# Performance work log

Measured on AMD Instinct MI355X. Metric: run time of the kernel, lower is better.

## Reference

```python
import jax, jax.numpy as jnp
import numpy as np

L = 5          # num_layer
D = 128        # emb_dim
N = 150000     # nodes
E = 500000     # edges
NF_ATOM, VA = 9, 119   # OGB atom feature count / max vocab
NF_BOND, VB = 3, 6     # OGB bond feature count / max vocab
BN_EPS = 1e-5


def setup_inputs() -> dict:
    key = jax.random.key(0)
    ks = jax.random.split(key, 10)
    s = 0.1
    x = jax.random.randint(ks[0], (N, NF_ATOM), 0, VA)
    edge_index = jax.random.randint(ks[1], (2, E), 0, N)
    edge_attr = jax.random.randint(ks[2], (E, NF_BOND), 0, VB)
    batch = jnp.sort(jax.random.randint(ks[3], (N,), 0, 2000))
    atom_emb = s * jax.random.normal(ks[4], (NF_ATOM, VA, D), dtype=jnp.float32)
    bond_emb = s * jax.random.normal(ks[5], (L, NF_BOND, VB, D), dtype=jnp.float32)
    eps = jnp.zeros((L,), jnp.float32)
    W1 = s * jax.random.normal(ks[6], (L, D, 2 * D), dtype=jnp.float32)
    b1 = jnp.zeros((L, 2 * D), jnp.float32)
    bn1_g = jnp.ones((L, 2 * D), jnp.float32)
    bn1_b = jnp.zeros((L, 2 * D), jnp.float32)
    W2 = s * jax.random.normal(ks[7], (L, 2 * D, D), dtype=jnp.float32)
    b2 = jnp.zeros((L, D), jnp.float32)
    bn_g = jnp.ones((L, D), jnp.float32)
    bn_b = jnp.zeros((L, D), jnp.float32)
    return dict(x=x, edge_index=edge_index, edge_attr=edge_attr, batch=batch,
                atom_emb=atom_emb, bond_emb=bond_emb, eps=eps,
                W1=W1, b1=b1, bn1_g=bn1_g, bn1_b=bn1_b,
                W2=W2, b2=b2, bn_g=bn_g, bn_b=bn_b)


def _bn(z, g, b):
    # BatchNorm1d with batch statistics (training-mode normalization)
    m = jnp.mean(z, axis=0)
    v = jnp.var(z, axis=0)
    return (z - m) * jax.lax.rsqrt(v + BN_EPS) * g + b


def _sum_embed(tables, idx):
    # tables: [F, V, D], idx: [n, F] -> sum_f tables[f][idx[:, f]] -> [n, D]
    return jax.vmap(lambda t, i: t[i], in_axes=(0, 1))(tables, idx).sum(0)


def reference(x, edge_index, edge_attr, batch, atom_emb, bond_emb, eps,
              W1, b1, bn1_g, bn1_b, W2, b2, bn_g, bn_b):
    n = x.shape[0]
    src, dst = edge_index[0], edge_index[1]
    h = _sum_embed(atom_emb, x)                      # AtomEncoder: [N, D]
    for l in range(L):
        e = _sum_embed(bond_emb[l], edge_attr)       # BondEncoder: [E, D]
        msg = jax.nn.relu(h[src] + e)                # message: gather + add + ReLU
        aggr = jax.ops.segment_sum(msg, dst, num_segments=n)  # scatter-add
        z = (1.0 + eps[l]) * h + aggr
        z = z @ W1[l] + b1[l]                        # [N, 2D]
        z = jax.nn.relu(_bn(z, bn1_g[l], bn1_b[l]))
        z = z @ W2[l] + b2[l]                        # [N, D]
        z = _bn(z, bn_g[l], bn_b[l])                 # outer BatchNorm
        if l < L - 1:
            z = jax.nn.relu(z)
        # dropout is identity in eval mode
        h = z + h                                    # residual
    return h  # JK='last'
```

## Files before the change

### kernel.cpp

```cpp
#include <hip/hip_runtime.h>

#define N_NODES 150000
#define N_EDGES 500000
#define D 128
#define D2 256
#define NLAYER 5
#define NB1 586
#define NROWT 9375
#define NBLK1 512
#define NBLK2 512

typedef __attribute__((ext_vector_type(8))) short bf16x8;
typedef __attribute__((ext_vector_type(4))) float f32x4;
typedef __attribute__((ext_vector_type(2))) float f32x2;
typedef __attribute__((ext_vector_type(4))) unsigned short ushort4v;
typedef __attribute__((ext_vector_type(8))) unsigned short ushort8v;
typedef __attribute__((ext_vector_type(4))) unsigned int u32x4;

__device__ __forceinline__ unsigned short f2bf(float f) {
    unsigned int u = __builtin_bit_cast(unsigned int, f);
    u += 0x7fffu + ((u >> 16) & 1u);
    return (unsigned short)(u >> 16);
}
__device__ __forceinline__ unsigned short f2bf_hw(float f) {
    return __builtin_bit_cast(unsigned short, (__bf16)f);
}
__device__ __forceinline__ float bf2f(unsigned short s) {
    unsigned int u = ((unsigned int)s) << 16;
    return __builtin_bit_cast(float, u);
}

__global__ __launch_bounds__(256) void prepw_kernel(const float* __restrict__ W1,
        const float* __restrict__ W2, unsigned short* __restrict__ w1t,
        unsigned short* __restrict__ w2t) {
    int i = blockIdx.x * 256 + threadIdx.x;
    if (i < NLAYER * D2 * D) {
        int l = i / (D2 * D);
        int rem = i % (D2 * D);
        int n = rem / D;
        int k = rem % D;
        w1t[i] = f2bf(W1[(l * D + k) * D2 + n]);
    }
    if (i < NLAYER * D * D2) {
        int l = i / (D * D2);
        int rem = i % (D * D2);
        int n = rem / D2;
        int k = rem % D2;
        w2t[i] = f2bf(W2[(l * D2 + k) * D + n]);
    }
}

__global__ __launch_bounds__(128) void combo_kernel(const float* __restrict__ bemb,
        float* __restrict__ combo) {
    int b = blockIdx.x;
    int l = b / 216, p = b % 216;
    int a0 = p % 6, a1 = (p / 6) % 6, a2 = p / 36;
    int d = threadIdx.x;
    combo[b * D + d] = bemb[((l * 3 + 0) * 6 + a0) * D + d]
                     + bemb[((l * 3 + 1) * 6 + a1) * D + d]
                     + bemb[((l * 3 + 2) * 6 + a2) * D + d];
}

__global__ __launch_bounds__(256) void atom_enc_kernel(const int* __restrict__ x,
        const float* __restrict__ aemb, unsigned short* __restrict__ hbf) {
    int node = blockIdx.x * 8 + (threadIdx.x >> 5);
    int t = threadIdx.x & 31;
    int d0 = t * 4;
    f32x4 s = {0, 0, 0, 0};
#pragma unroll
    for (int f = 0; f < 9; ++f) {
        int xi = x[node * 9 + f];
        f32x4 v = *(const f32x4*)(aemb + (size_t)(f * 119 + xi) * D + d0);
        s[0] += v[0]; s[1] += v[1]; s[2] += v[2]; s[3] += v[3];
    }
    ushort4v o;
#pragma unroll
    for (int j = 0; j < 4; ++j) o[j] = f2bf_hw(s[j]);
    *(ushort4v*)(hbf + (size_t)node * D + d0) = o;
}

__global__ __launch_bounds__(256) void hist_kernel(const int* __restrict__ ei,
        int* __restrict__ deg) {
    int e = blockIdx.x * 256 + threadIdx.x;
    if (e < N_EDGES) atomicAdd(&deg[ei[N_EDGES + e]], 1);
}

__global__ __launch_bounds__(256) void scan1_kernel(const int* __restrict__ deg,
        int* __restrict__ part, int* __restrict__ bsum) {
    __shared__ int sd[256];
    int tid = threadIdx.x;
    int i = blockIdx.x * 256 + tid;
    int v = (i < N_NODES) ? deg[i] : 0;
    sd[tid] = v;
    __syncthreads();
    for (int off = 1; off < 256; off <<= 1) {
        int t = (tid >= off) ? sd[tid - off] : 0;
        __syncthreads();
        sd[tid] += t;
        __syncthreads();
    }
    if (i < N_NODES) part[i] = sd[tid] - v;
    if (tid == 255) bsum[blockIdx.x] = sd[255];
}

__global__ __launch_bounds__(1024) void scan2_kernel(const int* __restrict__ bsum,
        int* __restrict__ boff) {
    __shared__ int sd[1024];
    int tid = threadIdx.x;
    int v = (tid < NB1) ? bsum[tid] : 0;
    sd[tid] = v;
    __syncthreads();
    for (int off = 1; off < 1024; off <<= 1) {
        int t = (tid >= off) ? sd[tid - off] : 0;
        __syncthreads();
        sd[tid] += t;
        __syncthreads();
    }
    if (tid < NB1) boff[tid] = sd[tid] - v;
}

__global__ __launch_bounds__(256) void scan3_kernel(const int* __restrict__ part,
        const int* __restrict__ boff, int* __restrict__ row_start) {
    int i = blockIdx.x * 256 + threadIdx.x;
    if (i < N_NODES) row_start[i] = part[i] + boff[i >> 8];
}

__global__ __launch_bounds__(256) void bin_kernel(const int* __restrict__ ei,
        const int* __restrict__ ea, const int* __restrict__ row_start,
        int* __restrict__ cursor, int* __restrict__ bins) {
    int e = blockIdx.x * 256 + threadIdx.x;
    if (e >= N_EDGES) return;
    int dst = ei[N_EDGES + e];
    int pos = row_start[dst] + atomicAdd(&cursor[dst], 1);
    int pack = ea[e * 3 + 0] + ea[e * 3 + 1] * 6 + ea[e * 3 + 2] * 36;
    bins[pos] = ei[e] | (pack << 18);
}

__global__ __launch_bounds__(256) void aggr_kernel(const int* __restrict__ row_start,
        const int* __restrict__ deg, const int* __restrict__ bins,
        const float* __restrict__ combo, const unsigned short* __restrict__ hbf,
        const float* __restrict__ epsp, unsigned short* __restrict__ A) {
    int wid = threadIdx.x >> 6;
    int lane = threadIdx.x & 63;
    int sub = lane >> 4;
    int t = lane & 15;
    int d0 = t * 8;
    int node = blockIdx.x * 16 + wid * 4 + sub;
    float ke = 1.0f + epsp[0];
    int start = row_start[node];
    int dg = deg[node];
    f32x4 s0 = {0, 0, 0, 0}, s1 = {0, 0, 0, 0};
    int entry = (dg > 0) ? bins[start] : 0;
    for (int i = 0; i < dg; ++i) {
        int next = (i + 1 < dg) ? bins[start + i + 1] : 0;
        int src = entry & 0x3FFFF;
        int pack = entry >> 18;
        ushort8v hv = *(const ushort8v*)(hbf + (size_t)src * D + d0);
        f32x4 c0 = *(const f32x4*)(combo + pack * D + d0);
        f32x4 c1 = *(const f32x4*)(combo + pack * D + d0 + 4);
#pragma unroll
        for (int j = 0; j < 4; ++j) {
            s0[j] += fmaxf(bf2f(hv[j]) + c0[j], 0.f);
            s1[j] += fmaxf(bf2f(hv[j + 4]) + c1[j], 0.f);
        }
        entry = next;
    }
    ushort8v hs = *(const ushort8v*)(hbf + (size_t)node * D + d0);
    ushort8v o;
#pragma unroll
    for (int j = 0; j < 4; ++j) {
        o[j]     = f2bf_hw(ke * bf2f(hs[j]) + s0[j]);
        o[j + 4] = f2bf_hw(ke * bf2f(hs[j + 4]) + s1[j]);
    }
    *(ushort8v*)(A + (size_t)node * D + d0) = o;
}

__global__ __launch_bounds__(256) void gemm1_kernel(const unsigned short* __restrict__ A,
        const unsigned short* __restrict__ w1t, const float* __restrict__ b1,
        unsigned short* __restrict__ z1, float* __restrict__ part1) {
    __shared__ unsigned short sm[4][16][76];
    int wave = threadIdx.x >> 6;
    int lane = threadIdx.x & 63;
    int l15 = lane & 15;
    int kg = lane >> 4;
    int rrow = lane >> 3;
    int rcol = (lane & 7) * 8;

    bf16x8 B[4][4];
    float bias[4];
#pragma unroll
    for (int t = 0; t < 4; ++t) {
        int col = (wave * 4 + t) * 16 + l15;
        bias[t] = b1[col];
#pragma unroll
        for (int kk = 0; kk < 4; ++kk)
            B[t][kk] = *(const bf16x8*)(w1t + (size_t)col * D + kk * 32 + kg * 8);
    }
    float s[4] = {0.f, 0.f, 0.f, 0.f}, q[4] = {0.f, 0.f, 0.f, 0.f};

    int rt = blockIdx.x;
    bf16x8 afn[4];
    {
        int row = rt * 16 + l15;
#pragma unroll
        for (int kk = 0; kk < 4; ++kk)
            afn[kk] = *(const bf16x8*)(A + (size_t)row * D + kk * 32 + kg * 8);
    }
    while (rt < NROWT) {
        int rtn = rt + NBLK1;
        bf16x8 af[4];
#pragma unroll
        for (int kk = 0; kk < 4; ++kk) af[kk] = afn[kk];
        if (rtn < NROWT) {
            int row = rtn * 16 + l15;
#pragma unroll
            for (int kk = 0; kk < 4; ++kk)
                afn[kk] = *(const bf16x8*)(A + (size_t)row * D + kk * 32 + kg * 8);
        }
        f32x4 acc[4];
#pragma unroll
        for (int t = 0; t < 4; ++t) acc[t] = (f32x4){0.f, 0.f, 0.f, 0.f};
#pragma unroll
        for (int kk = 0; kk < 4; ++kk)
#pragma unroll
            for (int t = 0; t < 4; ++t)
                acc[t] = __builtin_amdgcn_mfma_f32_16x16x32_bf16(af[kk], B[t][kk], acc[t], 0, 0, 0);
#pragma unroll
        for (int t = 0; t < 4; ++t) {
#pragma unroll
            for (int r = 0; r < 4; ++r) {
                float va = acc[t][r] + bias[t];
                s[t] += va;
                q[t] = fmaf(va, va, q[t]);
                sm[wave][kg * 4 + r][t * 16 + l15] = f2bf_hw(va);
            }
        }
        ushort8v v0 = *(const ushort8v*)&sm[wave][rrow][rcol];
        ushort8v v1 = *(const ushort8v*)&sm[wave][8 + rrow][rcol];
        *(ushort8v*)(z1 + (size_t)(rt * 16 + rrow) * D2 + wave * 64 + rcol) = v0;
        *(ushort8v*)(z1 + (size_t)(rt * 16 + 8 + rrow) * D2 + wave * 64 + rcol) = v1;
        rt = rtn;
    }
#pragma unroll
    for (int t = 0; t < 4; ++t) {
        s[t] += __shfl_xor(s[t], 16); s[t] += __shfl_xor(s[t], 32);
        q[t] += __shfl_xor(q[t], 16); q[t] += __shfl_xor(q[t], 32);
        if (kg == 0) {
            int col = (wave * 4 + t) * 16 + l15;
            part1[(size_t)blockIdx.x * 512 + col] = s[t];
            part1[(size_t)blockIdx.x * 512 + 256 + col] = q[t];
        }
    }
}

__global__ __launch_bounds__(256) void reduce_finalize_kernel(const float* __restrict__ part,
        int nblk, int C, const float* __restrict__ g, const float* __restrict__ bb,
        float* __restrict__ scale, float* __restrict__ shift,
        unsigned short* __restrict__ shpb) {
    int c = blockIdx.x;
    int tid = threadIdx.x;
    float s = 0.f, q = 0.f;
    for (int i = tid; i < nblk; i += 256) {
        s += part[(size_t)i * 2 * C + c];
        q += part[(size_t)i * 2 * C + C + c];
    }
#pragma unroll
    for (int off = 1; off < 64; off <<= 1) {
        s += __shfl_xor(s, off);
        q += __shfl_xor(q, off);
    }
    __shared__ float rs[4], rq[4];
    int w = tid >> 6;
    if ((tid & 63) == 0) { rs[w] = s; rq[w] = q; }
    __syncthreads();
    if (tid == 0) {
        s = rs[0] + rs[1] + rs[2] + rs[3];
        q = rq[0] + rq[1] + rq[2] + rq[3];
        float inv_n = 1.0f / (float)N_NODES;
        float mean = s * inv_n;
        float var = q * inv_n - mean * mean;
        float sc = g[c] * rsqrtf(var + 1e-5f);
        float sh = bb[c] - mean * sc;
        scale[c] = sc;
        shift[c] = sh;
        shpb[c] = f2bf(sh / sc);
    }
}

__global__ __launch_bounds__(256) void gemm2_kernel(const unsigned short* __restrict__ z1,
        const float* __restrict__ scale1, const unsigned short* __restrict__ shpb,
        const unsigned short* __restrict__ w2t, const float* __restrict__ b2,
        unsigned short* __restrict__ z2, float* __restrict__ part2) {
    __shared__ unsigned short sm2[4][16][44];
    int wave = threadIdx.x >> 6;
    int lane = threadIdx.x & 63;
    int l15 = lane & 15;
    int kg = lane >> 4;
    int rrow = lane >> 2;
    int rcol = (lane & 3) * 8;

    bf16x8 B[2][8];
    float bias[2];
#pragma unroll
    for (int t = 0; t < 2; ++t) {
        int col = (wave * 2 + t) * 16 + l15;
        bias[t] = b2[col];
#pragma unroll
        for (int kk = 0; kk < 8; ++kk) {
            bf16x8 raw = *(const bf16x8*)(w2t + (size_t)col * D2 + kk * 32 + kg * 8);
            int k0 = kk * 32 + kg * 8;
            const f32x4* sp = (const f32x4*)(scale1 + k0);
            f32x4 s0 = sp[0], s1 = sp[1];
            ushort8v bw;
#pragma unroll
            for (int j = 0; j < 4; ++j) {
                bw[j]     = f2bf_hw(bf2f((unsigned short)raw[j]) * s0[j]);
                bw[j + 4] = f2bf_hw(bf2f((unsigned short)raw[j + 4]) * s1[j]);
            }
            B[t][kk] = __builtin_bit_cast(bf16x8, bw);
        }
    }
    u32x4 shpu[8];
#pragma unroll
    for (int kk = 0; kk < 8; ++kk)
        shpu[kk] = *(const u32x4*)(shpb + kk * 32 + kg * 8);

    float s[2] = {0.f, 0.f}, q[2] = {0.f, 0.f};

    int rt = blockIdx.x;
    bf16x8 zrn[8];
    {
        int row = rt * 16 + l15;
#pragma unroll
        for (int kk = 0; kk < 8; ++kk)
            zrn[kk] = *(const bf16x8*)(z1 + (size_t)row * D2 + kk * 32 + kg * 8);
    }
    while (rt < NROWT) {
        int rtn = rt + NBLK2;
        bf16x8 a[8];
#pragma unroll
        for (int kk = 0; kk < 8; ++kk) {
            u32x4 zw = __builtin_bit_cast(u32x4, zrn[kk]);
            u32x4 pw = shpu[kk];
            ushort8v aw;
#pragma unroll
            for (int w = 0; w < 4; ++w) {
                float zlo = __builtin_bit_cast(float, zw[w] << 16);
                float zhi = __builtin_bit_cast(float, zw[w] & 0xffff0000u);
                float plo = __builtin_bit_cast(float, pw[w] << 16);
                float phi = __builtin_bit_cast(float, pw[w] & 0xffff0000u);
                aw[2 * w]     = f2bf_hw(fmaxf(zlo + plo, 0.f));
                aw[2 * w + 1] = f2bf_hw(fmaxf(zhi + phi, 0.f));
            }
            a[kk] = __builtin_bit_cast(bf16x8, aw);
        }
        if (rtn < NROWT) {
            int row = rtn * 16 + l15;
#pragma unroll
            for (int kk = 0; kk < 8; ++kk)
                zrn[kk] = *(const bf16x8*)(z1 + (size_t)row * D2 + kk * 32 + kg * 8);
        }
        f32x4 acc[2];
        acc[0] = (f32x4){0.f, 0.f, 0.f, 0.f};
        acc[1] = (f32x4){0.f, 0.f, 0.f, 0.f};
#pragma unroll
        for (int kk = 0; kk < 8; ++kk) {
            acc[0] = __builtin_amdgcn_mfma_f32_16x16x32_bf16(a[kk], B[0][kk], acc[0], 0, 0, 0);
            acc[1] = __builtin_amdgcn_mfma_f32_16x16x32_bf16(a[kk], B[1][kk], acc[1], 0, 0, 0);
        }
#pragma unroll
        for (int t = 0; t < 2; ++t) {
#pragma unroll
            for (int r = 0; r < 4; ++r) {
                float va = acc[t][r] + bias[t];
                s[t] += va;
                q[t] = fmaf(va, va, q[t]);
                sm2[wave][kg * 4 + r][t * 16 + l15] = f2bf_hw(va);
            }
        }
        ushort8v v0 = *(const ushort8v*)&sm2[wave][rrow][rcol];
        *(ushort8v*)(z2 + (size_t)(rt * 16 + rrow) * D + wave * 32 + rcol) = v0;
        rt = rtn;
    }
#pragma unroll
    for (int t = 0; t < 2; ++t) {
        s[t] += __shfl_xor(s[t], 16); s[t] += __shfl_xor(s[t], 32);
        q[t] += __shfl_xor(q[t], 16); q[t] += __shfl_xor(q[t], 32);
        if (kg == 0) {
            int col = (wave * 2 + t) * 16 + l15;
            part2[(size_t)blockIdx.x * 256 + col] = s[t];
            part2[(size_t)blockIdx.x * 256 + 128 + col] = q[t];
        }
    }
}

__global__ __launch_bounds__(256) void final_kernel(const unsigned short* __restrict__ z2,
        const float* __restrict__ scale, const float* __restrict__ shift,
        unsigned short* __restrict__ hbf, float* __restrict__ hout, int last) {
    int i = blockIdx.x * 256 + threadIdx.x;
    int base = i * 8;
    int c = base & (D - 1);
    f32x4 sc0 = *(const f32x4*)(scale + c);
    f32x4 sc1 = *(const f32x4*)(scale + c + 4);
    f32x4 sh0 = *(const f32x4*)(shift + c);
    f32x4 sh1 = *(const f32x4*)(shift + c + 4);
    ushort8v zv = *(const ushort8v*)(z2 + base);
    ushort8v hv = *(const ushort8v*)(hbf + base);
    if (last) {
        f32x4 o0, o1;
#pragma unroll
        for (int j = 0; j < 4; ++j) {
            o0[j] = fmaf(bf2f(zv[j]), sc0[j], sh0[j]) + bf2f(hv[j]);
            o1[j] = fmaf(bf2f(zv[j + 4]), sc1[j], sh1[j]) + bf2f(hv[j + 4]);
        }
        *(f32x4*)(hout + base) = o0;
        *(f32x4*)(hout + base + 4) = o1;
    } else {
        ushort8v ob;
#pragma unroll
        for (int j = 0; j < 4; ++j) {
            float v0 = fmaxf(fmaf(bf2f(zv[j]), sc0[j], sh0[j]), 0.f) + bf2f(hv[j]);
            float v1 = fmaxf(fmaf(bf2f(zv[j + 4]), sc1[j], sh1[j]), 0.f) + bf2f(hv[j + 4]);
            ob[j] = f2bf_hw(v0);
            ob[j + 4] = f2bf_hw(v1);
        }
        *(ushort8v*)(hbf + base) = ob;
    }
}

extern "C" void kernel_launch(void* const* d_in, const int* in_sizes, int n_in,
                              void* d_out, int out_size, void* d_ws, size_t ws_size,
                              hipStream_t stream) {
    const int* x = (const int*)d_in[0];
    const int* ei = (const int*)d_in[1];
    const int* ea = (const int*)d_in[2];
    const float* aemb = (const float*)d_in[4];
    const float* bemb = (const float*)d_in[5];
    const float* eps = (const float*)d_in[6];
    const float* W1 = (const float*)d_in[7];
    const float* b1 = (const float*)d_in[8];
    const float* bn1g = (const float*)d_in[9];
    const float* bn1b = (const float*)d_in[10];
    const float* W2 = (const float*)d_in[11];
    const float* b2 = (const float*)d_in[12];
    const float* bng = (const float*)d_in[13];
    const float* bnb = (const float*)d_in[14];
    float* h = (float*)d_out;

    char* ws = (char*)d_ws;
    size_t off = 0;
    auto alloc = [&](size_t bytes) {
        void* p = ws + off;
        off += (bytes + 255) & ~(size_t)255;
        return p;
    };
    unsigned short* z1  = (unsigned short*)alloc((size_t)N_NODES * D2 * 2);
    unsigned short* Az2 = (unsigned short*)alloc((size_t)N_NODES * D * 2);
    unsigned short* hbf = (unsigned short*)alloc((size_t)N_NODES * D * 2);
    unsigned short* w1t = (unsigned short*)alloc((size_t)NLAYER * D2 * D * 2);
    unsigned short* w2t = (unsigned short*)alloc((size_t)NLAYER * D * D2 * 2);
    float* combo        = (float*)alloc((size_t)NLAYER * 216 * D * 4);
    int* bins           = (int*)alloc((size_t)N_EDGES * 4);
    int* row_start      = (int*)alloc((size_t)(NB1 * 256) * 4);
    int* deg            = (int*)alloc((size_t)(NB1 * 256) * 4);
    int* cursor         = (int*)alloc((size_t)(NB1 * 256) * 4);
    int* part           = (int*)alloc((size_t)(NB1 * 256) * 4);
    int* bsum           = (int*)alloc(1024 * 4);
    int* boff           = (int*)alloc(1024 * 4);
    float* part1        = (float*)alloc((size_t)NBLK1 * 512 * 4);
    float* part2        = (float*)alloc((size_t)NBLK2 * 256 * 4);
    float* scale1 = (float*)alloc(256 * 4);
    float* shift1 = (float*)alloc(256 * 4);
    float* scale2 = (float*)alloc(128 * 4);
    float* shift2 = (float*)alloc(128 * 4);
    unsigned short* shp1 = (unsigned short*)alloc(256 * 2);
    unsigned short* shp2 = (unsigned short*)alloc(128 * 2);

    prepw_kernel<<<(NLAYER * D2 * D + 255) / 256, 256, 0, stream>>>(W1, W2, w1t, w2t);
    combo_kernel<<<NLAYER * 216, 128, 0, stream>>>(bemb, combo);
    atom_enc_kernel<<<N_NODES / 8, 256, 0, stream>>>(x, aemb, hbf);

    hipMemsetAsync(deg, 0, (size_t)(NB1 * 256) * 4, stream);
    hipMemsetAsync(cursor, 0, (size_t)(NB1 * 256) * 4, stream);
    hist_kernel<<<(N_EDGES + 255) / 256, 256, 0, stream>>>(ei, deg);
    scan1_kernel<<<NB1, 256, 0, stream>>>(deg, part, bsum);
    scan2_kernel<<<1, 1024, 0, stream>>>(bsum, boff);
    scan3_kernel<<<NB1, 256, 0, stream>>>(part, boff, row_start);
    bin_kernel<<<(N_EDGES + 255) / 256, 256, 0, stream>>>(ei, ea, row_start, cursor, bins);

    for (int l = 0; l < NLAYER; ++l) {
        aggr_kernel<<<N_NODES / 16, 256, 0, stream>>>(row_start, deg, bins,
                combo + l * 216 * D, hbf, eps + l, Az2);
        gemm1_kernel<<<NBLK1, 256, 0, stream>>>(Az2, w1t + l * D2 * D,
                b1 + l * D2, z1, part1);
        reduce_finalize_kernel<<<256, 256, 0, stream>>>(part1, NBLK1, D2,
                bn1g + l * D2, bn1b + l * D2, scale1, shift1, shp1);
        gemm2_kernel<<<NBLK2, 256, 0, stream>>>(z1, scale1, shp1,
                w2t + l * D * D2, b2 + l * D, Az2, part2);
        reduce_finalize_kernel<<<128, 256, 0, stream>>>(part2, NBLK2, D,
                bng + l * D, bnb + l * D, scale2, shift2, shp2);
        final_kernel<<<(N_NODES * D / 8) / 256, 256, 0, stream>>>(Az2, scale2, shift2,
                hbf, h, (l == NLAYER - 1) ? 1 : 0);
    }
}
```

Before: 764.8 us.

## Fuse GEMM1 recompute into GEMM2 to drop the z1 round-trip through HBM

The first GEMM pass now only computes the BatchNorm statistics and no longer stores the [N,256] bf16 intermediate. A new fused kernel recomputes GEMM1 per 16-row tile, applies the bias, folded shift and ReLU, stages the result in shared memory, and feeds it straight into GEMM2. This removes the large z1 write and read each layer. The cost is running GEMM1 twice and two block barriers per row tile, and z1 is no longer rounded to bf16 before the shift is added.

```diff
diff --git a/kernel.cpp b/kernel.cpp
--- a/kernel.cpp
+++ b/kernel.cpp
@@ -12,7 +12,6 @@
 
 typedef __attribute__((ext_vector_type(8))) short bf16x8;
 typedef __attribute__((ext_vector_type(4))) float f32x4;
-typedef __attribute__((ext_vector_type(2))) float f32x2;
 typedef __attribute__((ext_vector_type(4))) unsigned short ushort4v;
 typedef __attribute__((ext_vector_type(8))) unsigned short ushort8v;
 typedef __attribute__((ext_vector_type(4))) unsigned int u32x4;
@@ -175,16 +174,13 @@
     *(ushort8v*)(A + (size_t)node * D + d0) = o;
 }
 
-__global__ __launch_bounds__(256) void gemm1_kernel(const unsigned short* __restrict__ A,
+__global__ __launch_bounds__(256) void gemm1s_kernel(const unsigned short* __restrict__ A,
         const unsigned short* __restrict__ w1t, const float* __restrict__ b1,
-        unsigned short* __restrict__ z1, float* __restrict__ part1) {
-    __shared__ unsigned short sm[4][16][76];
+        float* __restrict__ part1) {
     int wave = threadIdx.x >> 6;
     int lane = threadIdx.x & 63;
     int l15 = lane & 15;
     int kg = lane >> 4;
-    int rrow = lane >> 3;
-    int rcol = (lane & 7) * 8;
 
     bf16x8 B[4][4];
     float bias[4];
@@ -232,13 +228,8 @@
                 float va = acc[t][r] + bias[t];
                 s[t] += va;
                 q[t] = fmaf(va, va, q[t]);
-                sm[wave][kg * 4 + r][t * 16 + l15] = f2bf_hw(va);
             }
         }
-        ushort8v v0 = *(const ushort8v*)&sm[wave][rrow][rcol];
-        ushort8v v1 = *(const ushort8v*)&sm[wave][8 + rrow][rcol];
-        *(ushort8v*)(z1 + (size_t)(rt * 16 + rrow) * D2 + wave * 64 + rcol) = v0;
-        *(ushort8v*)(z1 + (size_t)(rt * 16 + 8 + rrow) * D2 + wave * 64 + rcol) = v1;
         rt = rtn;
     }
 #pragma unroll
@@ -287,10 +278,12 @@
     }
 }
 
-__global__ __launch_bounds__(256) void gemm2_kernel(const unsigned short* __restrict__ z1,
-        const float* __restrict__ scale1, const unsigned short* __restrict__ shpb,
+__global__ __launch_bounds__(256) void gemm12_kernel(const unsigned short* __restrict__ A,
+        const unsigned short* __restrict__ w1t, const float* __restrict__ b1,
+        const unsigned short* __restrict__ shpb, const float* __restrict__ scale1,
         const unsigned short* __restrict__ w2t, const float* __restrict__ b2,
         unsigned short* __restrict__ z2, float* __restrict__ part2) {
+    __shared__ unsigned short z1t[16][264];
     __shared__ unsigned short sm2[4][16][44];
     int wave = threadIdx.x >> 6;
     int lane = threadIdx.x & 63;
@@ -299,12 +292,22 @@
     int rrow = lane >> 2;
     int rcol = (lane & 3) * 8;
 
-    bf16x8 B[2][8];
-    float bias[2];
+    bf16x8 B1[4][4];
+    float bs1[4];
+#pragma unroll
+    for (int t = 0; t < 4; ++t) {
+        int col = (wave * 4 + t) * 16 + l15;
+        bs1[t] = b1[col] + bf2f(shpb[col]);
+#pragma unroll
+        for (int kk = 0; kk < 4; ++kk)
+            B1[t][kk] = *(const bf16x8*)(w1t + (size_t)col * D + kk * 32 + kg * 8);
+    }
+    bf16x8 B2[2][8];
+    float bias2[2];
 #pragma unroll
     for (int t = 0; t < 2; ++t) {
         int col = (wave * 2 + t) * 16 + l15;
-        bias[t] = b2[col];
+        bias2[t] = b2[col];
 #pragma unroll
         for (int kk = 0; kk < 8; ++kk) {
             bf16x8 raw = *(const bf16x8*)(w2t + (size_t)col * D2 + kk * 32 + kg * 8);
@@ -317,62 +320,62 @@
                 bw[j]     = f2bf_hw(bf2f((unsigned short)raw[j]) * s0[j]);
                 bw[j + 4] = f2bf_hw(bf2f((unsigned short)raw[j + 4]) * s1[j]);
             }
-            B[t][kk] = __builtin_bit_cast(bf16x8, bw);
-        }
-    }
-    u32x4 shpu[8];
-#pragma unroll
-    for (int kk = 0; kk < 8; ++kk)
-        shpu[kk] = *(const u32x4*)(shpb + kk * 32 + kg * 8);
+            B2[t][kk] = __builtin_bit_cast(bf16x8, bw);
+        }
+    }
 
     float s[2] = {0.f, 0.f}, q[2] = {0.f, 0.f};
 
     int rt = blockIdx.x;
-    bf16x8 zrn[8];
+    bf16x8 afn[4];
     {
         int row = rt * 16 + l15;
 #pragma unroll
-        for (int kk = 0; kk < 8; ++kk)
-            zrn[kk] = *(const bf16x8*)(z1 + (size_t)row * D2 + kk * 32 + kg * 8);
+        for (int kk = 0; kk < 4; ++kk)
+            afn[kk] = *(const bf16x8*)(A + (size_t)row * D + kk * 32 + kg * 8);
     }
     while (rt < NROWT) {
         int rtn = rt + NBLK2;
-        bf16x8 a[8];
-#pragma unroll
-        for (int kk = 0; kk < 8; ++kk) {
-            u32x4 zw = __builtin_bit_cast(u32x4, zrn[kk]);
-            u32x4 pw = shpu[kk];
-            ushort8v aw;
-#pragma unroll
-            for (int w = 0; w < 4; ++w) {
-                float zlo = __builtin_bit_cast(float, zw[w] << 16);
-                float zhi = __builtin_bit_cast(float, zw[w] & 0xffff0000u);
-                float plo = __builtin_bit_cast(float, pw[w] << 16);
-                float phi = __builtin_bit_cast(float, pw[w] & 0xffff0000u);
-                aw[2 * w]     = f2bf_hw(fmaxf(zlo + plo, 0.f));
-                aw[2 * w + 1] = f2bf_hw(fmaxf(zhi + phi, 0.f));
-            }
-            a[kk] = __builtin_bit_cast(bf16x8, aw);
-        }
+        bf16x8 af[4];
+#pragma unroll
+        for (int kk = 0; kk < 4; ++kk) af[kk] = afn[kk];
         if (rtn < NROWT) {
             int row = rtn * 16 + l15;
 #pragma unroll
-            for (int kk = 0; kk < 8; ++kk)
-                zrn[kk] = *(const bf16x8*)(z1 + (size_t)row * D2 + kk * 32 + kg * 8);
-        }
-        f32x4 acc[2];
-        acc[0] = (f32x4){0.f, 0.f, 0.f, 0.f};
-        acc[1] = (f32x4){0.f, 0.f, 0.f, 0.f};
+            for (int kk = 0; kk < 4; ++kk)
+                afn[kk] = *(const bf16x8*)(A + (size_t)row * D + kk * 32 + kg * 8);
+        }
+        f32x4 acc1[4];
+#pragma unroll
+        for (int t = 0; t < 4; ++t) acc1[t] = (f32x4){0.f, 0.f, 0.f, 0.f};
+#pragma unroll
+        for (int kk = 0; kk < 4; ++kk)
+#pragma unroll
+            for (int t = 0; t < 4; ++t)
+                acc1[t] = __builtin_amdgcn_mfma_f32_16x16x32_bf16(af[kk], B1[t][kk], acc1[t], 0, 0, 0);
+        __syncthreads();
+#pragma unroll
+        for (int t = 0; t < 4; ++t) {
+            int col = (wave * 4 + t) * 16 + l15;
+#pragma unroll
+            for (int r = 0; r < 4; ++r)
+                z1t[kg * 4 + r][col] = f2bf_hw(fmaxf(acc1[t][r] + bs1[t], 0.f));
+        }
+        __syncthreads();
+        f32x4 acc2[2];
+        acc2[0] = (f32x4){0.f, 0.f, 0.f, 0.f};
+        acc2[1] = (f32x4){0.f, 0.f, 0.f, 0.f};
 #pragma unroll
         for (int kk = 0; kk < 8; ++kk) {
-            acc[0] = __builtin_amdgcn_mfma_f32_16x16x32_bf16(a[kk], B[0][kk], acc[0], 0, 0, 0);
-            acc[1] = __builtin_amdgcn_mfma_f32_16x16x32_bf16(a[kk], B[1][kk], acc[1], 0, 0, 0);
+            bf16x8 a2 = __builtin_bit_cast(bf16x8, *(const ushort8v*)&z1t[l15][kk * 32 + kg * 8]);
+            acc2[0] = __builtin_amdgcn_mfma_f32_16x16x32_bf16(a2, B2[0][kk], acc2[0], 0, 0, 0);
+            acc2[1] = __builtin_amdgcn_mfma_f32_16x16x32_bf16(a2, B2[1][kk], acc2[1], 0, 0, 0);
         }
 #pragma unroll
         for (int t = 0; t < 2; ++t) {
 #pragma unroll
             for (int r = 0; r < 4; ++r) {
-                float va = acc[t][r] + bias[t];
+                float va = acc2[t][r] + bias2[t];
                 s[t] += va;
                 q[t] = fmaf(va, va, q[t]);
                 sm2[wave][kg * 4 + r][t * 16 + l15] = f2bf_hw(va);
@@ -454,7 +457,6 @@
         off += (bytes + 255) & ~(size_t)255;
         return p;
     };
-    unsigned short* z1  = (unsigned short*)alloc((size_t)N_NODES * D2 * 2);
     unsigned short* Az2 = (unsigned short*)alloc((size_t)N_NODES * D * 2);
     unsigned short* hbf = (unsigned short*)alloc((size_t)N_NODES * D * 2);
     unsigned short* w1t = (unsigned short*)alloc((size_t)NLAYER * D2 * D * 2);
@@ -491,12 +493,12 @@
     for (int l = 0; l < NLAYER; ++l) {
         aggr_kernel<<<N_NODES / 16, 256, 0, stream>>>(row_start, deg, bins,
                 combo + l * 216 * D, hbf, eps + l, Az2);
-        gemm1_kernel<<<NBLK1, 256, 0, stream>>>(Az2, w1t + l * D2 * D,
-                b1 + l * D2, z1, part1);
+        gemm1s_kernel<<<NBLK1, 256, 0, stream>>>(Az2, w1t + l * D2 * D,
+                b1 + l * D2, part1);
         reduce_finalize_kernel<<<256, 256, 0, stream>>>(part1, NBLK1, D2,
                 bn1g + l * D2, bn1b + l * D2, scale1, shift1, shp1);
-        gemm2_kernel<<<NBLK2, 256, 0, stream>>>(z1, scale1, shp1,
-                w2t + l * D * D2, b2 + l * D, Az2, part2);
+        gemm12_kernel<<<NBLK2, 256, 0, stream>>>(Az2, w1t + l * D2 * D,
+                b1 + l * D2, shp1, scale1, w2t + l * D * D2, b2 + l * D, Az2, part2);
         reduce_finalize_kernel<<<128, 256, 0, stream>>>(part2, NBLK2, D,
                 bng + l * D, bnb + l * D, scale2, shift2, shp2);
         final_kernel<<<(N_NODES * D / 8) / 256, 256, 0, stream>>>(Az2, scale2, shift2,
```

New measurement: 714.7 us, median of 2. -6.6%, faster.
